# Kernel tuning notes

Measured on AMD Instinct MI355X. Metric: run time of the kernel, lower is better.

## Reference

```python
import jax, jax.numpy as jnp
import numpy as np

B = 2          # batch
S = 4096       # byte-level sequence length
D = 512        # d_hidden_bytelevel
BPL = 4        # bytes_per_latent
H = 16         # n_attention_heads
DQK = 64       # d_qkv_bytelevel (== rope d_hidden)
DLAT = 1024    # d_hidden_latent
LQ = S // BPL  # latent sequence length
EPS = 1.1920929e-07  # torch RMSNorm default eps = float32 finfo eps
ROPE_BASE = 10000.0


def _rope(x, pos):
    # x: [B, H, L, DQK], pos: [L] float positions. Half-split rotation.
    half = DQK // 2
    inv_freq = ROPE_BASE ** (-jnp.arange(half, dtype=jnp.float32) / half)  # [half]
    ang = pos[:, None] * inv_freq[None, :]                                 # [L, half]
    cos, sin = jnp.cos(ang), jnp.sin(ang)
    x1, x2 = x[..., :half], x[..., half:]
    return jnp.concatenate([x1 * cos - x2 * sin, x1 * sin + x2 * cos], axis=-1)


def setup_inputs() -> dict:
    key = jax.random.key(0)
    ks = jax.random.split(key, 9)
    s = 0.02
    return {
        "x": jax.random.normal(ks[0], (B, S, D), dtype=jnp.float32),
        "norm_w": jnp.ones((D,), dtype=jnp.float32),
        "wq_w": jax.random.normal(ks[1], (BPL * D, H * DQK), dtype=jnp.float32) * s,
        "wq_b": jax.random.normal(ks[2], (H * DQK,), dtype=jnp.float32) * s,
        "wkv_w": jax.random.normal(ks[3], (D, 2 * H * DQK), dtype=jnp.float32) * s,
        "wkv_b": jax.random.normal(ks[4], (2 * H * DQK,), dtype=jnp.float32) * s,
        "wout_w": jax.random.normal(ks[5], (H * DQK, DLAT), dtype=jnp.float32) * s,
        "wout_b": jax.random.normal(ks[6], (DLAT,), dtype=jnp.float32) * s,
        "wbyp_w": jax.random.normal(ks[7], (BPL * D, DLAT), dtype=jnp.float32) * s,
    }


def reference(x, norm_w, wq_w, wq_b, wkv_w, wkv_b, wout_w, wout_b, wbyp_w):
    # RMSNorm (elementwise affine)
    normalized = x * jax.lax.rsqrt(jnp.mean(x * x, axis=-1, keepdims=True) + EPS) * norm_w
    # merge groups of BPL bytes -> latent query tokens: [B, LQ, BPL*D]
    merged = normalized.reshape(B, LQ, BPL * D)
    # fused Q projection: [B, H, LQ, DQK]
    q = (merged @ wq_w + wq_b).reshape(B, LQ, H, DQK).transpose(0, 2, 1, 3)
    # merged KV projection: split dim first, then heads -> [B, S, 2, H, DQK]
    kv = (normalized @ wkv_w + wkv_b).reshape(B, S, 2, H, DQK)
    k = kv[:, :, 0].transpose(0, 2, 1, 3)  # [B, H, S, DQK]
    v = kv[:, :, 1].transpose(0, 2, 1, 3)
    # strided RoPE for Q (positions i*BPL), unit-stride for K
    q = _rope(q, jnp.arange(LQ, dtype=jnp.float32) * BPL)
    k = _rope(k, jnp.arange(S, dtype=jnp.float32))
    # SDPA (non-causal)
    scores = jnp.einsum('bhqd,bhkd->bhqk', q, k) * (1.0 / np.sqrt(DQK).astype(np.float32))
    attn = jax.nn.softmax(scores, axis=-1)
    attn_out = jnp.einsum('bhqk,bhkd->bhqd', attn, v)
    attn_concat = attn_out.transpose(0, 2, 1, 3).reshape(B, LQ, H * DQK)
    out = attn_concat @ wout_w + wout_b
    # bypass: raw x grouped by BPL, bias-free projection
    bypass = x.reshape(B, LQ, BPL * D) @ wbyp_w
    return out + bypass
```

## Files before the change

kernel.cpp:

```cpp
#include <hip/hip_runtime.h>

using u16 = unsigned short;
using u32 = unsigned int;

typedef __attribute__((ext_vector_type(8))) short bf16x8;
typedef __attribute__((ext_vector_type(8))) unsigned short u16x8;
typedef __attribute__((ext_vector_type(4))) float f32x4;
typedef __attribute__((ext_vector_type(16))) float f32x16;
typedef __attribute__((ext_vector_type(4))) u32 u32x4;

constexpr int Bb   = 2;
constexpr int Ss   = 4096;
constexpr int Dd   = 512;
constexpr int Hh   = 16;
constexpr int DQK  = 64;
constexpr int LQ   = 1024;
constexpr int DLAT = 1024;

#define QSCL 0.18033688011112042f

__device__ __forceinline__ u16 f2bf(float f){
  u32 u = __float_as_uint(f);
  u += 0x7FFFu + ((u >> 16) & 1u);
  return (u16)(u >> 16);
}
__device__ __forceinline__ u32 permpack(float hi, float lo){
  return __builtin_amdgcn_perm(__float_as_uint(hi), __float_as_uint(lo), 0x07060302u);
}

#define GLDS16(gp, lp) \
  __builtin_amdgcn_global_load_lds((const __attribute__((address_space(1))) u32*)(gp), \
                                   (__attribute__((address_space(3))) u32*)(lp), 16, 0, 0)

__global__ __launch_bounds__(256) void rmsnorm_kernel(
    const float* __restrict__ x, const float* __restrict__ w,
    u16* __restrict__ normb, u16* __restrict__ xb)
{
  const int lane = threadIdx.x & 63;
  const int row  = blockIdx.x * 4 + (threadIdx.x >> 6);
  const float4* xr = (const float4*)(x + (size_t)row * Dd);
  float4 a = xr[lane*2], b2 = xr[lane*2 + 1];
  float ss = a.x*a.x + a.y*a.y + a.z*a.z + a.w*a.w
           + b2.x*b2.x + b2.y*b2.y + b2.z*b2.z + b2.w*b2.w;
  #pragma unroll
  for (int off = 1; off < 64; off <<= 1) ss += __shfl_xor(ss, off);
  const float sc = rsqrtf(ss * (1.0f / Dd) + 1.1920929e-07f);
  const int c0 = lane * 8;
  const float4* wr4 = (const float4*)(w + c0);
  float4 w0 = wr4[0], w1 = wr4[1];
  u16x8 nv, xv;
  nv[0]=f2bf(a.x *sc*w0.x); nv[1]=f2bf(a.y *sc*w0.y); nv[2]=f2bf(a.z *sc*w0.z); nv[3]=f2bf(a.w *sc*w0.w);
  nv[4]=f2bf(b2.x*sc*w1.x); nv[5]=f2bf(b2.y*sc*w1.y); nv[6]=f2bf(b2.z*sc*w1.z); nv[7]=f2bf(b2.w*sc*w1.w);
  xv[0]=f2bf(a.x);  xv[1]=f2bf(a.y);  xv[2]=f2bf(a.z);  xv[3]=f2bf(a.w);
  xv[4]=f2bf(b2.x); xv[5]=f2bf(b2.y); xv[6]=f2bf(b2.z); xv[7]=f2bf(b2.w);
  *(u16x8*)(normb + (size_t)row * Dd + c0) = nv;
  *(u16x8*)(xb    + (size_t)row * Dd + c0) = xv;
}

__global__ __launch_bounds__(256) void rope_tab_kernel(float2* __restrict__ tab){
  int i = blockIdx.x * 256 + threadIdx.x;
  int pos = i >> 5, d = i & 31;
  float inv = exp2f(-(float)d * 0.41524101186092028f);
  float ang = (float)pos * inv;
  float s, c;
  sincosf(ang, &s, &c);
  tab[i] = make_float2(c, s);
}

__global__ __launch_bounds__(256) void transpose_cast_kernel(
    const float* __restrict__ W, u16* __restrict__ Wt,
    int N, int ldt, int koff)
{
  __shared__ float t[64][65];
  const int k0 = blockIdx.x * 64, n0 = blockIdx.y * 64;
  const int c = threadIdx.x & 63, r0 = threadIdx.x >> 6;
  #pragma unroll
  for (int i = 0; i < 16; ++i){
    int r = i*4 + r0;
    t[r][c] = W[(size_t)(k0 + r) * N + n0 + c];
  }
  __syncthreads();
  #pragma unroll
  for (int i = 0; i < 16; ++i){
    int r = i*4 + r0;
    Wt[(size_t)(n0 + r) * ldt + koff + k0 + c] = f2bf(t[c][r]);
  }
}

__device__ __forceinline__ void gemm_core64(
    const u16* __restrict__ A, int lda,
    const u16* __restrict__ Bt, int ldb, int kofs,
    int K, int bm0, int bn0, char* lds,
    f32x4 (&acc)[4])
{
  const int tid = threadIdx.x, lane = tid & 63, w = tid >> 6;
  const int l15 = lane & 15, l4 = lane >> 4;

  #pragma unroll
  for (int j = 0; j < 4; ++j) acc[j] = (f32x4){0.f, 0.f, 0.f, 0.f};

  auto stage = [&](int t){
    char* dst = lds + (t % 3) * 16384;
    const int k0 = t * 64;
    #pragma unroll
    for (int i = 0; i < 4; ++i){
      int u = i*256 + tid;
      int row = u >> 3;
      int colb = ((u & 7) * 16) ^ ((row & 7) << 4);
      const u16* src = (row < 64)
        ? A  + (size_t)(bm0 + row) * lda + k0 + (colb >> 1)
        : Bt + (size_t)(bn0 + row - 64) * ldb + kofs + k0 + (colb >> 1);
      GLDS16(src, dst + u*16);
    }
  };

  const int nt = K >> 6;
  stage(0);
  if (nt > 1) stage(1);

  #pragma unroll 1
  for (int t = 0; t < nt; ++t){
    if (t + 1 < nt) { asm volatile("s_waitcnt vmcnt(4)" ::: "memory"); }
    else            { asm volatile("s_waitcnt vmcnt(0)" ::: "memory"); }
    __builtin_amdgcn_sched_barrier(0);
    __builtin_amdgcn_s_barrier();

    const char* kb = lds + (t % 3) * 16384;
    bf16x8 af[2], bf[4][2];
    #pragma unroll
    for (int ks = 0; ks < 2; ++ks){
      const int row = w*16 + l15;
      af[ks] = *(const bf16x8*)(kb + row*128 + ((ks*64 + l4*16) ^ ((row & 7) << 4)));
    }
    #pragma unroll
    for (int j = 0; j < 4; ++j)
      #pragma unroll
      for (int ks = 0; ks < 2; ++ks){
        const int row = 64 + j*16 + l15;
        bf[j][ks] = *(const bf16x8*)(kb + row*128 + ((ks*64 + l4*16) ^ ((row & 7) << 4)));
      }
    asm volatile("s_waitcnt lgkmcnt(0)" ::: "memory");
    __builtin_amdgcn_sched_barrier(0);
    if (t + 2 < nt) stage(t + 2);

    __builtin_amdgcn_s_setprio(1);
    #pragma unroll
    for (int ks = 0; ks < 2; ++ks)
      #pragma unroll
      for (int j = 0; j < 4; ++j)
        acc[j] = __builtin_amdgcn_mfma_f32_16x16x32_bf16(af[ks], bf[j][ks], acc[j], 0, 0, 0);
    __builtin_amdgcn_s_setprio(0);
  }
}

__global__ __launch_bounds__(256, 3) void qkv_kernel(
    const u16* __restrict__ normb,
    const u16* __restrict__ wtq, const u16* __restrict__ wtkv,
    const float* __restrict__ wq_b, const float* __restrict__ wkv_b,
    const float2* __restrict__ rtab,
    u16* __restrict__ Qb, u16* __restrict__ Kb, u16* __restrict__ Vtb)
{
  __shared__ char lds[49152];
  const int bid = blockIdx.x;
  const int lane = threadIdx.x & 63, w = threadIdx.x >> 6;
  const int ml = (lane >> 4) * 4, nl = lane & 15;
  f32x4 acc[4];

  if (bid < 512){
    const int bm0 = (bid & 31) * 64, bn0 = (bid >> 5) * 64;
    gemm_core64(normb, 2048, wtq, 2048, 0, 2048, bm0, bn0, lds, acc);
    const int h = bn0 >> 6;
    #pragma unroll
    for (int j = 0; j < 2; ++j){
      const int d1 = j*16 + nl;
      const float b1 = wq_b[bn0 + j*16 + nl], b2v = wq_b[bn0 + (j+2)*16 + nl];
      #pragma unroll
      for (int r = 0; r < 4; ++r){
        int m = bm0 + w*16 + ml + r;
        int b = m >> 10, lq = m & 1023;
        float x1 = acc[j][r] + b1;
        float x2 = acc[j+2][r] + b2v;
        float2 cs = rtab[(lq*4)*32 + d1];
        size_t ob = ((size_t)(b*Hh + h) * LQ + lq) * DQK;
        Qb[ob + d1]      = f2bf((x1*cs.x - x2*cs.y) * QSCL);
        Qb[ob + d1 + 32] = f2bf((x1*cs.y + x2*cs.x) * QSCL);
      }
    }
  } else {
    const int t = bid - 512;
    const int bm0 = (t & 127) * 64, bn0 = (t >> 7) * 64;
    gemm_core64(normb, 512, wtkv, 512, 0, 512, bm0, bn0, lds, acc);
    const int kv = bn0 >> 10;
    const int h = (bn0 & 1023) >> 6;
    const int m0 = bm0 + w*16 + ml;
    const int b = m0 >> 12, s = m0 & 4095;
    if (kv == 0){
      #pragma unroll
      for (int r = 0; r < 4; ++r){
        size_t ob = ((size_t)(b*Hh + h) * Ss + s + r) * DQK;
        #pragma unroll
        for (int j = 0; j < 2; ++j){
          int d1 = j*16 + nl;
          float x1 = acc[j][r]   + wkv_b[bn0 + j*16 + nl];
          float x2 = acc[j+2][r] + wkv_b[bn0 + (j+2)*16 + nl];
          float2 cs = rtab[(s+r)*32 + d1];
          Kb[ob + d1]      = f2bf(x1*cs.x - x2*cs.y);
          Kb[ob + d1 + 32] = f2bf(x1*cs.y + x2*cs.x);
        }
      }
    } else {
      #pragma unroll
      for (int j = 0; j < 4; ++j){
        const int d = j*16 + nl;
        const float bb = wkv_b[bn0 + d];
        uint2 pv;
        pv.x = permpack(acc[j][1] + bb, acc[j][0] + bb);
        pv.y = permpack(acc[j][3] + bb, acc[j][2] + bb);
        *(uint2*)(Vtb + (((size_t)(b*Hh + h)) * DQK + d) * Ss + s) = pv;
      }
    }
  }
}

__global__ __launch_bounds__(256, 3) void out_kernel(
    const u16* __restrict__ ACb, const u16* __restrict__ xb,
    const u16* __restrict__ wto, const float* __restrict__ wout_b,
    float* __restrict__ outp)
{
  __shared__ char lds[49152];
  const int bm0 = blockIdx.x * 64, bn0 = blockIdx.y * 64;
  const int lane = threadIdx.x & 63, w = threadIdx.x >> 6;
  const int ml = (lane >> 4) * 4, nl = lane & 15;
  f32x4 acc[4], acc2[4];
  gemm_core64(ACb, 1024, wto, 3072, 0,    1024, bm0, bn0, lds, acc);
  __syncthreads();
  gemm_core64(xb,  2048, wto, 3072, 1024, 2048, bm0, bn0, lds, acc2);
  #pragma unroll
  for (int j = 0; j < 4; ++j){
    const int n = bn0 + j*16 + nl;
    const float bb = wout_b[n];
    #pragma unroll
    for (int r = 0; r < 4; ++r){
      int m = bm0 + w*16 + ml + r;
      outp[(size_t)m * DLAT + n] = acc[j][r] + acc2[j][r] + bb;
    }
  }
}

__global__ __launch_bounds__(512, 2) void flash_kernel(
    const u16* __restrict__ Qg, const u16* __restrict__ Kg,
    const u16* __restrict__ Vtg, float* __restrict__ Opart,
    float* __restrict__ lpart)
{
  const int tid = threadIdx.x, lane = tid & 63, w = tid >> 6;
  const int bid = blockIdx.x;
  const int swz = (bid & 7) * 32 + (bid >> 3);
  const int sq = swz & 3, qh = (swz >> 2) & 1, bh = swz >> 3;
  const int sbase = sq * 1024;
  const int l31 = lane & 31, hgl = lane >> 5;

  __shared__ char lds[49152];

  bf16x8 qf[2][4];
  #pragma unroll
  for (int qt = 0; qt < 2; ++qt)
    #pragma unroll
    for (int ks = 0; ks < 4; ++ks)
      qf[qt][ks] = *(const bf16x8*)(Qg + ((size_t)bh*LQ + qh*512 + w*64 + qt*32 + l31) * DQK + ks*16 + hgl*8);

  f32x16 o[2][2];
  #pragma unroll
  for (int qt = 0; qt < 2; ++qt)
    #pragma unroll
    for (int nd = 0; nd < 2; ++nd)
      #pragma unroll
      for (int r = 0; r < 16; ++r) o[qt][nd][r] = 0.f;
  float l_run[2] = {0.f, 0.f};

  auto stage = [&](int t){
    char* dst = lds + (t % 3) * 16384;
    const int s0 = sbase + t * 64;
    #pragma unroll
    for (int i = 0; i < 2; ++i){
      int u = (w*2 + i) * 64 + lane;
      int row = (u >> 3) & 63;
      int colb = ((u & 7) * 16) ^ ((row & 7) << 4);
      const u16* src = (u < 512)
          ? Kg  + ((size_t)bh*Ss  + s0 + row) * DQK + (colb >> 1)
          : Vtg + ((size_t)bh*DQK + row) * Ss + s0  + (colb >> 1);
      GLDS16(src, dst + u*16);
    }
  };

  stage(0);
  stage(1);

  #pragma unroll 1
  for (int t = 0; t < 16; ++t){
    if (t < 15) { asm volatile("s_waitcnt vmcnt(2)" ::: "memory"); }
    else        { asm volatile("s_waitcnt vmcnt(0)" ::: "memory"); }
    __builtin_amdgcn_sched_barrier(0);
    __builtin_amdgcn_s_barrier();

    const char* kb = lds + (t % 3) * 16384;
    bf16x8 kf[2][4], vf[2][4];
    #pragma unroll
    for (int kvt = 0; kvt < 2; ++kvt)
      #pragma unroll
      for (int ks = 0; ks < 4; ++ks){
        const int row = kvt*32 + l31;
        kf[kvt][ks] = *(const bf16x8*)(kb + row*128 + ((ks*32 + hgl*16) ^ ((row & 7) << 4)));
      }
    #pragma unroll
    for (int nd = 0; nd < 2; ++nd)
      #pragma unroll
      for (int k2 = 0; k2 < 4; ++k2){
        const int row = nd*32 + l31;
        vf[nd][k2] = *(const bf16x8*)(kb + 8192 + row*128 + ((k2*32 + hgl*16) ^ ((row & 7) << 4)));
      }
    asm volatile("s_waitcnt lgkmcnt(0)" ::: "memory");
    __builtin_amdgcn_sched_barrier(0);
    if (t < 14) stage(t + 2);

    #pragma unroll
    for (int qt = 0; qt < 2; ++qt){
      f32x16 sc[2];
      #pragma unroll
      for (int kvt = 0; kvt < 2; ++kvt)
        #pragma unroll
        for (int r = 0; r < 16; ++r) sc[kvt][r] = 0.f;
      __builtin_amdgcn_s_setprio(1);
      #pragma unroll
      for (int kvt = 0; kvt < 2; ++kvt)
        #pragma unroll
        for (int ks = 0; ks < 4; ++ks)
          sc[kvt] = __builtin_amdgcn_mfma_f32_32x32x16_bf16(kf[kvt][ks], qf[qt][ks], sc[kvt], 0, 0, 0);
      __builtin_amdgcn_s_setprio(0);

      float s_loc = 0.f;
      u32x4 paw[4];
      #pragma unroll
      for (int kvt = 0; kvt < 2; ++kvt){
        #pragma unroll
        for (int r = 0; r < 16; ++r){
          float p = __builtin_amdgcn_exp2f(sc[kvt][r]);
          sc[kvt][r] = p;
          s_loc += p;
        }
        #pragma unroll
        for (int k2r = 0; k2r < 2; ++k2r){
          u32 a0 = permpack(sc[kvt][k2r*8+1], sc[kvt][k2r*8+0]);
          u32 a1 = permpack(sc[kvt][k2r*8+3], sc[kvt][k2r*8+2]);
          u32 a2 = permpack(sc[kvt][k2r*8+5], sc[kvt][k2r*8+4]);
          u32 a3 = permpack(sc[kvt][k2r*8+7], sc[kvt][k2r*8+6]);
          asm("v_permlane32_swap_b32 %0, %1" : "+v"(a0), "+v"(a2));
          asm("v_permlane32_swap_b32 %0, %1" : "+v"(a1), "+v"(a3));
          const int k2 = kvt*2 + k2r;
          paw[k2][0] = a0; paw[k2][1] = a1;
          paw[k2][2] = a2; paw[k2][3] = a3;
        }
      }
      l_run[qt] += s_loc;

      __builtin_amdgcn_s_setprio(1);
      #pragma unroll
      for (int nd = 0; nd < 2; ++nd)
        #pragma unroll
        for (int k2 = 0; k2 < 4; ++k2)
          o[qt][nd] = __builtin_amdgcn_mfma_f32_32x32x16_bf16(
              __builtin_bit_cast(bf16x8, paw[k2]), vf[nd][k2], o[qt][nd], 0, 0, 0);
      __builtin_amdgcn_s_setprio(0);
    }
  }

  #pragma unroll
  for (int qt = 0; qt < 2; ++qt){
    float lf = l_run[qt] + __shfl_xor(l_run[qt], 32);
    float* Ob = Opart + ((size_t)sq * 32768 + (size_t)bh * 1024) * 64;
    #pragma unroll
    for (int nd = 0; nd < 2; ++nd)
      #pragma unroll
      for (int r = 0; r < 16; ++r){
        int q = qh*512 + w*64 + qt*32 + (r & 3) + 8*(r >> 2) + 4*hgl;
        Ob[(size_t)q * 64 + nd*32 + l31] = o[qt][nd][r];
      }
    if (hgl == 0)
      lpart[(size_t)sq * 32768 + (size_t)bh * 1024 + qh*512 + w*64 + qt*32 + l31] = lf;
  }
}

__global__ __launch_bounds__(256) void merge_kernel(
    const float* __restrict__ Opart, const float* __restrict__ lpart,
    u16* __restrict__ AC)
{
  int idx = blockIdx.x * 256 + threadIdx.x;
  int row = idx >> 3, dg = idx & 7;
  int bh = row >> 10, lq = row & 1023;
  int b = bh >> 4, h = bh & 15;
  float a[8];
  #pragma unroll
  for (int e = 0; e < 8; ++e) a[e] = 0.f;
  float lt = 0.f;
  #pragma unroll
  for (int p = 0; p < 4; ++p){
    const float4* pp = (const float4*)(Opart + ((size_t)p * 32768 + row) * 64 + dg * 8);
    float4 v0 = pp[0], v1 = pp[1];
    a[0]+=v0.x; a[1]+=v0.y; a[2]+=v0.z; a[3]+=v0.w;
    a[4]+=v1.x; a[5]+=v1.y; a[6]+=v1.z; a[7]+=v1.w;
    lt += lpart[(size_t)p * 32768 + row];
  }
  float rl = 1.0f / lt;
  u16x8 r;
  #pragma unroll
  for (int e = 0; e < 8; ++e) r[e] = f2bf(a[e] * rl);
  *(u16x8*)(AC + ((size_t)(b*LQ + lq)) * (Hh*DQK) + h*DQK + dg*8) = r;
}

extern "C" void kernel_launch(void* const* d_in, const int* in_sizes, int n_in,
                              void* d_out, int out_size, void* d_ws, size_t ws_size,
                              hipStream_t stream)
{
  (void)in_sizes; (void)n_in; (void)out_size; (void)ws_size;
  const float* x      = (const float*)d_in[0];
  const float* norm_w = (const float*)d_in[1];
  const float* wq_w   = (const float*)d_in[2];
  const float* wq_b   = (const float*)d_in[3];
  const float* wkv_w  = (const float*)d_in[4];
  const float* wkv_b  = (const float*)d_in[5];
  const float* wout_w = (const float*)d_in[6];
  const float* wout_b = (const float*)d_in[7];
  const float* wbyp_w = (const float*)d_in[8];
  float* outp = (float*)d_out;

  char* p = (char*)d_ws;
  u16* normb = (u16*)p; p += (size_t)8192*512*2;
  u16* xb    = (u16*)p; p += (size_t)8192*512*2;
  u16* wtq   = (u16*)p; p += (size_t)1024*2048*2;
  u16* wtkv  = (u16*)p; p += (size_t)2048*512*2;
  u16* wto   = (u16*)p; p += (size_t)1024*3072*2;
  u16* Qb    = (u16*)p; p += (size_t)32*1024*64*2;
  u16* Kb    = (u16*)p; p += (size_t)32*4096*64*2;
  u16* Vtb   = (u16*)p; p += (size_t)32*64*4096*2;
  u16* ACb   = (u16*)p; p += (size_t)2048*1024*2;
  float2* rtab = (float2*)p; p += (size_t)4096*32*sizeof(float2);
  float* Opart = (float*)p; p += (size_t)4*32768*64*4;
  float* lpart = (float*)p; p += (size_t)4*32768*4;

  rmsnorm_kernel<<<2048, 256, 0, stream>>>(x, norm_w, normb, xb);
  rope_tab_kernel<<<512, 256, 0, stream>>>(rtab);
  transpose_cast_kernel<<<dim3(32,16), 256, 0, stream>>>(wq_w,   wtq,  1024, 2048, 0);
  transpose_cast_kernel<<<dim3(8,32),  256, 0, stream>>>(wkv_w,  wtkv, 2048, 512,  0);
  transpose_cast_kernel<<<dim3(16,16), 256, 0, stream>>>(wout_w, wto,  1024, 3072, 0);
  transpose_cast_kernel<<<dim3(32,16), 256, 0, stream>>>(wbyp_w, wto,  1024, 3072, 1024);

  qkv_kernel<<<4608, 256, 0, stream>>>(normb, wtq, wtkv, wq_b, wkv_b, rtab, Qb, Kb, Vtb);
  flash_kernel<<<256, 512, 0, stream>>>(Qb, Kb, Vtb, Opart, lpart);
  merge_kernel<<<1024, 256, 0, stream>>>(Opart, lpart, ACb);
  out_kernel<<<dim3(32,16), 256, 0, stream>>>(ACb, xb, wto, wout_b, outp);
}
```

Baseline: 137.7 us.

## Enlarge GEMM tiles to 128x128 and fuse out/bypass K loops

Result: slower. 160.5 us (+16.5%).

```diff
diff --git a/kernel.cpp b/kernel.cpp
--- a/kernel.cpp
+++ b/kernel.cpp
@@ -87,29 +87,37 @@
   }
 }
 
-__device__ __forceinline__ void gemm_core64(
+__device__ __forceinline__ void gemm_core128(
     const u16* __restrict__ A, int lda,
-    const u16* __restrict__ Bt, int ldb, int kofs,
+    const u16* __restrict__ A2, int lda2, int ksplit,
+    const u16* __restrict__ Bt, int ldb,
     int K, int bm0, int bn0, char* lds,
-    f32x4 (&acc)[4])
+    f32x4 (&acc)[4][4])
 {
   const int tid = threadIdx.x, lane = tid & 63, w = tid >> 6;
+  const int wr = w >> 1, wc = w & 1;
   const int l15 = lane & 15, l4 = lane >> 4;
 
   #pragma unroll
-  for (int j = 0; j < 4; ++j) acc[j] = (f32x4){0.f, 0.f, 0.f, 0.f};
+  for (int i = 0; i < 4; ++i)
+    #pragma unroll
+    for (int j = 0; j < 4; ++j) acc[i][j] = (f32x4){0.f, 0.f, 0.f, 0.f};
 
   auto stage = [&](int t){
-    char* dst = lds + (t % 3) * 16384;
+    char* dst = lds + (t % 3) * 32768;
     const int k0 = t * 64;
     #pragma unroll
-    for (int i = 0; i < 4; ++i){
+    for (int i = 0; i < 8; ++i){
       int u = i*256 + tid;
       int row = u >> 3;
       int colb = ((u & 7) * 16) ^ ((row & 7) << 4);
-      const u16* src = (row < 64)
-        ? A  + (size_t)(bm0 + row) * lda + k0 + (colb >> 1)
-        : Bt + (size_t)(bn0 + row - 64) * ldb + kofs + k0 + (colb >> 1);
+      const u16* src;
+      if (row < 128){
+        if (k0 < ksplit) src = A  + (size_t)(bm0 + row) * lda  + k0 + (colb >> 1);
+        else             src = A2 + (size_t)(bm0 + row) * lda2 + (k0 - ksplit) + (colb >> 1);
+      } else {
+        src = Bt + (size_t)(bn0 + row - 128) * ldb + k0 + (colb >> 1);
+      }
       GLDS16(src, dst + u*16);
     }
   };
@@ -120,23 +128,25 @@
 
   #pragma unroll 1
   for (int t = 0; t < nt; ++t){
-    if (t + 1 < nt) { asm volatile("s_waitcnt vmcnt(4)" ::: "memory"); }
+    if (t + 1 < nt) { asm volatile("s_waitcnt vmcnt(8)" ::: "memory"); }
     else            { asm volatile("s_waitcnt vmcnt(0)" ::: "memory"); }
     __builtin_amdgcn_sched_barrier(0);
     __builtin_amdgcn_s_barrier();
 
-    const char* kb = lds + (t % 3) * 16384;
-    bf16x8 af[2], bf[4][2];
-    #pragma unroll
-    for (int ks = 0; ks < 2; ++ks){
-      const int row = w*16 + l15;
-      af[ks] = *(const bf16x8*)(kb + row*128 + ((ks*64 + l4*16) ^ ((row & 7) << 4)));
-    }
+    const char* kb = lds + (t % 3) * 32768;
+    bf16x8 af[4][2], bf[4][2];
+    #pragma unroll
+    for (int i = 0; i < 4; ++i)
+      #pragma unroll
+      for (int ks = 0; ks < 2; ++ks){
+        const int row = wr*64 + i*16 + l15;
+        af[i][ks] = *(const bf16x8*)(kb + row*128 + ((ks*64 + l4*16) ^ ((row & 7) << 4)));
+      }
     #pragma unroll
     for (int j = 0; j < 4; ++j)
       #pragma unroll
       for (int ks = 0; ks < 2; ++ks){
-        const int row = 64 + j*16 + l15;
+        const int row = 128 + wc*64 + j*16 + l15;
         bf[j][ks] = *(const bf16x8*)(kb + row*128 + ((ks*64 + l4*16) ^ ((row & 7) << 4)));
       }
     asm volatile("s_waitcnt lgkmcnt(0)" ::: "memory");
@@ -147,104 +157,116 @@
     #pragma unroll
     for (int ks = 0; ks < 2; ++ks)
       #pragma unroll
-      for (int j = 0; j < 4; ++j)
-        acc[j] = __builtin_amdgcn_mfma_f32_16x16x32_bf16(af[ks], bf[j][ks], acc[j], 0, 0, 0);
+      for (int i = 0; i < 4; ++i)
+        #pragma unroll
+        for (int j = 0; j < 4; ++j)
+          acc[i][j] = __builtin_amdgcn_mfma_f32_16x16x32_bf16(af[i][ks], bf[j][ks], acc[i][j], 0, 0, 0);
     __builtin_amdgcn_s_setprio(0);
   }
 }
 
-__global__ __launch_bounds__(256, 3) void qkv_kernel(
+__global__ __launch_bounds__(256, 1) void qkv_kernel(
     const u16* __restrict__ normb,
     const u16* __restrict__ wtq, const u16* __restrict__ wtkv,
     const float* __restrict__ wq_b, const float* __restrict__ wkv_b,
     const float2* __restrict__ rtab,
     u16* __restrict__ Qb, u16* __restrict__ Kb, u16* __restrict__ Vtb)
 {
-  __shared__ char lds[49152];
+  __shared__ char lds[98304];
   const int bid = blockIdx.x;
   const int lane = threadIdx.x & 63, w = threadIdx.x >> 6;
+  const int wr = w >> 1, wc = w & 1;
   const int ml = (lane >> 4) * 4, nl = lane & 15;
-  f32x4 acc[4];
-
-  if (bid < 512){
-    const int bm0 = (bid & 31) * 64, bn0 = (bid >> 5) * 64;
-    gemm_core64(normb, 2048, wtq, 2048, 0, 2048, bm0, bn0, lds, acc);
-    const int h = bn0 >> 6;
-    #pragma unroll
-    for (int j = 0; j < 2; ++j){
-      const int d1 = j*16 + nl;
-      const float b1 = wq_b[bn0 + j*16 + nl], b2v = wq_b[bn0 + (j+2)*16 + nl];
-      #pragma unroll
-      for (int r = 0; r < 4; ++r){
-        int m = bm0 + w*16 + ml + r;
-        int b = m >> 10, lq = m & 1023;
-        float x1 = acc[j][r] + b1;
-        float x2 = acc[j+2][r] + b2v;
-        float2 cs = rtab[(lq*4)*32 + d1];
-        size_t ob = ((size_t)(b*Hh + h) * LQ + lq) * DQK;
-        Qb[ob + d1]      = f2bf((x1*cs.x - x2*cs.y) * QSCL);
-        Qb[ob + d1 + 32] = f2bf((x1*cs.y + x2*cs.x) * QSCL);
+  f32x4 acc[4][4];
+
+  if (bid < 128){
+    const int bm0 = (bid & 15) * 128, bn0 = (bid >> 4) * 128;
+    gemm_core128(normb, 2048, normb, 2048, 2048, wtq, 2048, 2048, bm0, bn0, lds, acc);
+    const int nbase = bn0 + wc*64;
+    const int h = nbase >> 6;
+    #pragma unroll
+    for (int i = 0; i < 4; ++i){
+      #pragma unroll
+      for (int j = 0; j < 2; ++j){
+        const int d1 = j*16 + nl;
+        const float b1 = wq_b[nbase + j*16 + nl], b2v = wq_b[nbase + (j+2)*16 + nl];
+        #pragma unroll
+        for (int r = 0; r < 4; ++r){
+          int m = bm0 + wr*64 + i*16 + ml + r;
+          int b = m >> 10, lq = m & 1023;
+          float x1 = acc[i][j][r] + b1;
+          float x2 = acc[i][j+2][r] + b2v;
+          float2 cs = rtab[(lq*4)*32 + d1];
+          size_t ob = ((size_t)(b*Hh + h) * LQ + lq) * DQK;
+          Qb[ob + d1]      = f2bf((x1*cs.x - x2*cs.y) * QSCL);
+          Qb[ob + d1 + 32] = f2bf((x1*cs.y + x2*cs.x) * QSCL);
+        }
       }
     }
   } else {
-    const int t = bid - 512;
-    const int bm0 = (t & 127) * 64, bn0 = (t >> 7) * 64;
-    gemm_core64(normb, 512, wtkv, 512, 0, 512, bm0, bn0, lds, acc);
-    const int kv = bn0 >> 10;
-    const int h = (bn0 & 1023) >> 6;
-    const int m0 = bm0 + w*16 + ml;
-    const int b = m0 >> 12, s = m0 & 4095;
-    if (kv == 0){
-      #pragma unroll
-      for (int r = 0; r < 4; ++r){
-        size_t ob = ((size_t)(b*Hh + h) * Ss + s + r) * DQK;
-        #pragma unroll
-        for (int j = 0; j < 2; ++j){
-          int d1 = j*16 + nl;
-          float x1 = acc[j][r]   + wkv_b[bn0 + j*16 + nl];
-          float x2 = acc[j+2][r] + wkv_b[bn0 + (j+2)*16 + nl];
-          float2 cs = rtab[(s+r)*32 + d1];
-          Kb[ob + d1]      = f2bf(x1*cs.x - x2*cs.y);
-          Kb[ob + d1 + 32] = f2bf(x1*cs.y + x2*cs.x);
+    const int t = bid - 128;
+    const int bm0 = (t & 63) * 128, bn0 = (t >> 6) * 128;
+    gemm_core128(normb, 512, normb, 512, 512, wtkv, 512, 512, bm0, bn0, lds, acc);
+    const int nbase = bn0 + wc*64;
+    const int kv = nbase >> 10;
+    const int h = (nbase & 1023) >> 6;
+    #pragma unroll
+    for (int i = 0; i < 4; ++i){
+      const int m0 = bm0 + wr*64 + i*16 + ml;
+      const int b = m0 >> 12, s = m0 & 4095;
+      if (kv == 0){
+        #pragma unroll
+        for (int r = 0; r < 4; ++r){
+          size_t ob = ((size_t)(b*Hh + h) * Ss + s + r) * DQK;
+          #pragma unroll
+          for (int j = 0; j < 2; ++j){
+            int d1 = j*16 + nl;
+            float x1 = acc[i][j][r]   + wkv_b[nbase + j*16 + nl];
+            float x2 = acc[i][j+2][r] + wkv_b[nbase + (j+2)*16 + nl];
+            float2 cs = rtab[(s+r)*32 + d1];
+            Kb[ob + d1]      = f2bf(x1*cs.x - x2*cs.y);
+            Kb[ob + d1 + 32] = f2bf(x1*cs.y + x2*cs.x);
+          }
         }
-      }
-    } else {
-      #pragma unroll
-      for (int j = 0; j < 4; ++j){
-        const int d = j*16 + nl;
-        const float bb = wkv_b[bn0 + d];
-        uint2 pv;
-        pv.x = permpack(acc[j][1] + bb, acc[j][0] + bb);
-        pv.y = permpack(acc[j][3] + bb, acc[j][2] + bb);
-        *(uint2*)(Vtb + (((size_t)(b*Hh + h)) * DQK + d) * Ss + s) = pv;
-      }
-    }
-  }
-}
-
-__global__ __launch_bounds__(256, 3) void out_kernel(
+      } else {
+        #pragma unroll
+        for (int j = 0; j < 4; ++j){
+          const int d = j*16 + nl;
+          const float bb = wkv_b[nbase + d];
+          uint2 pv;
+          pv.x = permpack(acc[i][j][1] + bb, acc[i][j][0] + bb);
+          pv.y = permpack(acc[i][j][3] + bb, acc[i][j][2] + bb);
+          *(uint2*)(Vtb + (((size_t)(b*Hh + h)) * DQK + d) * Ss + s) = pv;
+        }
+      }
+    }
+  }
+}
+
+__global__ __launch_bounds__(256, 1) void out_kernel(
     const u16* __restrict__ ACb, const u16* __restrict__ xb,
     const u16* __restrict__ wto, const float* __restrict__ wout_b,
     float* __restrict__ outp)
 {
-  __shared__ char lds[49152];
-  const int bm0 = blockIdx.x * 64, bn0 = blockIdx.y * 64;
+  __shared__ char lds[98304];
+  const int bm0 = blockIdx.x * 128, bn0 = blockIdx.y * 128;
   const int lane = threadIdx.x & 63, w = threadIdx.x >> 6;
+  const int wr = w >> 1, wc = w & 1;
   const int ml = (lane >> 4) * 4, nl = lane & 15;
-  f32x4 acc[4], acc2[4];
-  gemm_core64(ACb, 1024, wto, 3072, 0,    1024, bm0, bn0, lds, acc);
-  __syncthreads();
-  gemm_core64(xb,  2048, wto, 3072, 1024, 2048, bm0, bn0, lds, acc2);
-  #pragma unroll
-  for (int j = 0; j < 4; ++j){
-    const int n = bn0 + j*16 + nl;
-    const float bb = wout_b[n];
-    #pragma unroll
-    for (int r = 0; r < 4; ++r){
-      int m = bm0 + w*16 + ml + r;
-      outp[(size_t)m * DLAT + n] = acc[j][r] + acc2[j][r] + bb;
-    }
-  }
+  f32x4 acc[4][4];
+  gemm_core128(ACb, 1024, xb, 2048, 1024, wto, 3072, 3072, bm0, bn0, lds, acc);
+  #pragma unroll
+  for (int i = 0; i < 4; ++i)
+    #pragma unroll
+    for (int j = 0; j < 4; ++j){
+      const int n = bn0 + wc*64 + j*16 + nl;
+      const float bb = wout_b[n];
+      #pragma unroll
+      for (int r = 0; r < 4; ++r){
+        int m = bm0 + wr*64 + i*16 + ml + r;
+        outp[(size_t)m * DLAT + n] = acc[i][j][r] + bb;
+      }
+    }
 }
 
 __global__ __launch_bounds__(512, 2) void flash_kernel(
@@ -453,8 +475,8 @@
   transpose_cast_kernel<<<dim3(16,16), 256, 0, stream>>>(wout_w, wto,  1024, 3072, 0);
   transpose_cast_kernel<<<dim3(32,16), 256, 0, stream>>>(wbyp_w, wto,  1024, 3072, 1024);
 
-  qkv_kernel<<<4608, 256, 0, stream>>>(normb, wtq, wtkv, wq_b, wkv_b, rtab, Qb, Kb, Vtb);
+  qkv_kernel<<<1152, 256, 0, stream>>>(normb, wtq, wtkv, wq_b, wkv_b, rtab, Qb, Kb, Vtb);
   flash_kernel<<<256, 512, 0, stream>>>(Qb, Kb, Vtb, Opart, lpart);
   merge_kernel<<<1024, 256, 0, stream>>>(Opart, lpart, ACb);
-  out_kernel<<<dim3(32,16), 256, 0, stream>>>(ACb, xb, wto, wout_b, outp);
-}
+  out_kernel<<<dim3(16,8), 256, 0, stream>>>(ACb, xb, wto, wout_b, outp);
+}
```
